# Performance work log

Hardware: AMD Instinct MI355X
Metric: run time of the kernel (lower is better)

The kernel has to match this reference:

```python
import jax, jax.numpy as jnp
import numpy as np
from jax import lax

ITER_TIME = 32
DECAY = 0.9


def setup_inputs() -> dict:
    key = jax.random.key(0)
    k1, k2, k3, k4 = jax.random.split(key, 4)
    B, D_in, N, D_out = 256, 1024, 4096, 256
    s_in = 1.0 / np.sqrt(D_in)
    s_rec = 0.5 / np.sqrt(N)  # keep recurrence stable
    s_out = 1.0 / np.sqrt(N)
    return {
        "x": jax.random.normal(k1, (B, D_in), dtype=jnp.float32),
        "W_i": jax.random.normal(k2, (D_in, N), dtype=jnp.float32) * s_in,
        "b": jnp.zeros((N,), dtype=jnp.float32),
        "W_r": jax.random.normal(k3, (N, N), dtype=jnp.float32) * s_rec,
        "W_f": jax.random.normal(k4, (N, D_out), dtype=jnp.float32) * s_out,
    }


def reference(x, W_i, b, W_r, W_f):
    # prep_input_endure: constant input drive each timestep
    i_ = x @ W_i + b  # [B, N]
    u0 = jnp.zeros_like(i_)
    r0 = jnp.zeros_like(i_)

    def step(carry, _):
        u, r = carry
        u_new = DECAY * u + i_ + r           # leaky integration of drive + recurrent feedback
        a = jax.nn.relu(u_new)               # firing rate / surrogate spike
        r_new = a @ W_r                      # recurrent N->N feedback
        f = a @ W_f                          # readout N->Y
        return (u_new, r_new), (f, u_new)

    (_, _), (fs, us) = lax.scan(step, (u0, r0), None, length=ITER_TIME)
    output = jnp.transpose(fs, (1, 0, 2))  # [B, T, output_num]
    act = jnp.transpose(us, (1, 0, 2))     # [B, T, N_num]
    return output, act
```

## Files before the change

kernel.cpp:

```cpp
#include <hip/hip_runtime.h>
#include <hip/hip_bf16.h>

#define ITER_TIME 32
#define DECAY 0.9f

typedef __attribute__((ext_vector_type(8))) short short8;
typedef __attribute__((ext_vector_type(4))) float f32x4;
typedef __attribute__((ext_vector_type(4))) short short4v;
typedef unsigned short ushort_t;
typedef unsigned int u32;

__device__ __forceinline__ void gload16(const ushort_t* g, ushort_t* l) {
    __builtin_amdgcn_global_load_lds(
        (const __attribute__((address_space(1))) u32*)g,
        (__attribute__((address_space(3))) u32*)l, 16, 0, 0);
}

__global__ void conv_f32_bf16(const float* __restrict__ in,
                              __hip_bfloat16* __restrict__ out, int n) {
    int i = blockIdx.x * 256 + threadIdx.x;
    if (i < n) out[i] = __float2bfloat16(in[i]);
}

__global__ void transpose_f32_bf16(const float* __restrict__ in,
                                   __hip_bfloat16* __restrict__ out, int R,
                                   int C) {
    __shared__ float tile[32][33];
    int tx = threadIdx.x, ty = threadIdx.y;
    size_t x = blockIdx.x * 32 + tx;
    size_t y = blockIdx.y * 32 + ty;
    tile[ty][tx] = in[y * C + x];
    __syncthreads();
    size_t ox = blockIdx.y * 32 + tx;
    size_t oy = blockIdx.x * 32 + ty;
    out[oy * R + ox] = __float2bfloat16(tile[tx][ty]);
}

__global__ __launch_bounds__(256)
void gemm_wi(const ushort_t* __restrict__ A,
             const ushort_t* __restrict__ BT,
             const float* __restrict__ bias, float* __restrict__ i_,
             float* __restrict__ u, __hip_bfloat16* __restrict__ a0,
             float* __restrict__ act, int K) {
    __shared__ __attribute__((aligned(16))) ushort_t As[2][128 * 64];
    __shared__ __attribute__((aligned(16))) ushort_t Bs[2][128 * 64];

    int m0 = blockIdx.x * 128;
    int by = blockIdx.y;
    const ushort_t* Bsrc = BT + (size_t)by * 128 * K;

    int t = threadIdx.x;
    int wave = t >> 6, lane = t & 63;
    int quad = lane >> 4, l16 = lane & 15;
    int wm = (wave >> 1) * 64, wn = (wave & 1) * 64;

    int lr = lane >> 3;
    int lcol = ((lane & 7) ^ lr) << 3;
    const ushort_t* aBase = A + (size_t)(m0 + wave * 32 + lr) * K + lcol;
    const ushort_t* bBase = Bsrc + (size_t)(wave * 32 + lr) * K + lcol;

    f32x4 acc[4][4];
#pragma unroll
    for (int i = 0; i < 4; i++)
#pragma unroll
        for (int j = 0; j < 4; j++) acc[i][j] = (f32x4){0.f, 0.f, 0.f, 0.f};

    int nt = K >> 6;
    int swz = (l16 & 7) << 3;

    auto stage = [&](int buf, int kk) {
#pragma unroll
        for (int i = 0; i < 4; ++i) {
            gload16(aBase + (size_t)(i * 8) * K + kk,
                    &As[buf][(wave * 4 + i) * 512]);
            gload16(bBase + (size_t)(i * 8) * K + kk,
                    &Bs[buf][(wave * 4 + i) * 512]);
        }
    };

    stage(0, 0);
    __syncthreads();
    int cur = 0;
    for (int it = 0; it < nt; ++it) {
        if (it + 1 < nt) stage(cur ^ 1, (it + 1) * 64);
#pragma unroll
        for (int kstep = 0; kstep < 2; ++kstep) {
            int ko = kstep * 32 + quad * 8;
            int pc = ko ^ swz;
            short8 af[4], bfr[4];
#pragma unroll
            for (int i = 0; i < 4; i++)
                af[i] = *(const short8*)&As[cur][(wm + i * 16 + l16) * 64 + pc];
#pragma unroll
            for (int j = 0; j < 4; j++)
                bfr[j] = *(const short8*)&Bs[cur][(wn + j * 16 + l16) * 64 + pc];
#pragma unroll
            for (int i = 0; i < 4; i++)
#pragma unroll
                for (int j = 0; j < 4; j++)
                    acc[i][j] = __builtin_amdgcn_mfma_f32_16x16x32_bf16(
                        af[i], bfr[j], acc[i][j], 0, 0, 0);
        }
        __syncthreads();
        cur ^= 1;
    }

#pragma unroll
    for (int i = 0; i < 4; i++)
#pragma unroll
        for (int j = 0; j < 4; j++) {
            int gcol = by * 128 + wn + j * 16 + l16;
#pragma unroll
            for (int rr = 0; rr < 4; ++rr) {
                int grow = m0 + wm + i * 16 + quad * 4 + rr;
                size_t p = (size_t)grow * 4096 + gcol;
                float iv = acc[i][j][rr] + bias[gcol];
                i_[p] = iv;
                u[p] = iv;
                __builtin_nontemporal_store(
                    iv, &act[(size_t)grow * (ITER_TIME * 4096) + gcol]);
                float ar = iv > 0.f ? iv : 0.f;
                a0[p] = __float2bfloat16(ar);
            }
        }
}

template <int ONLY_F>
__global__ __launch_bounds__(256)
void gemm_step(const ushort_t* __restrict__ A,
               const ushort_t* __restrict__ BT,
               float* __restrict__ rp,
               float* __restrict__ fp) {
    const int K = 4096, klen = 1024;
    __shared__ __attribute__((aligned(16))) ushort_t As[2][128 * 64];
    __shared__ __attribute__((aligned(16))) ushort_t Bs[2][64 * 64];

    int blk = blockIdx.x;
    int by, w;
    if (ONLY_F) {
        by = 64 + (blk >> 3);
        w = blk & 7;
    } else if (blk < 512) {
        int xcd = blk & 7, bg = (blk >> 3) & 7;
        w = blk >> 6;
        by = xcd + 8 * bg;
    } else {
        int idx = blk - 512;
        by = 64 + (idx >> 3);
        w = idx & 7;
    }
    int m = w & 1, ks = w >> 1;
    int m0 = m * 128;
    const ushort_t* Bsrc = BT + (size_t)by * 64 * K;

    int tid = threadIdx.x;
    int wave = tid >> 6, lane = tid & 63;
    int quad = lane >> 4, l16 = lane & 15;
    int wm = (wave >> 1) * 64, wn = (wave & 1) * 32;

    int lr = lane >> 3;
    int lcol = ((lane & 7) ^ lr) << 3;
    const ushort_t* aBase = A + (size_t)(m0 + wave * 32 + lr) * K + lcol;
    const ushort_t* bBase = Bsrc + (size_t)(wave * 16 + lr) * K + lcol;

    f32x4 acc[4][2];
#pragma unroll
    for (int i = 0; i < 4; i++)
#pragma unroll
        for (int j = 0; j < 2; j++) acc[i][j] = (f32x4){0.f, 0.f, 0.f, 0.f};

    const int k0 = ks * klen;
    const int nt = klen >> 6;
    int swz = (l16 & 7) << 3;

    auto stage = [&](int buf, int kk) {
#pragma unroll
        for (int i = 0; i < 4; ++i)
            gload16(aBase + (size_t)(i * 8) * K + kk,
                    &As[buf][(wave * 4 + i) * 512]);
#pragma unroll
        for (int i = 0; i < 2; ++i)
            gload16(bBase + (size_t)(i * 8) * K + kk,
                    &Bs[buf][(wave * 2 + i) * 512]);
    };

    stage(0, k0);
    __syncthreads();
    int cur = 0;
    for (int it = 0; it < nt; ++it) {
        if (it + 1 < nt) stage(cur ^ 1, k0 + (it + 1) * 64);
#pragma unroll
        for (int kstep = 0; kstep < 2; ++kstep) {
            int ko = kstep * 32 + quad * 8;
            int pc = ko ^ swz;
            short8 af[4], bfr[2];
#pragma unroll
            for (int i = 0; i < 4; i++)
                af[i] = *(const short8*)&As[cur][(wm + i * 16 + l16) * 64 + pc];
#pragma unroll
            for (int j = 0; j < 2; j++)
                bfr[j] = *(const short8*)&Bs[cur][(wn + j * 16 + l16) * 64 + pc];
#pragma unroll
            for (int i = 0; i < 4; i++)
#pragma unroll
                for (int j = 0; j < 2; j++)
                    acc[i][j] = __builtin_amdgcn_mfma_f32_16x16x32_bf16(
                        af[i], bfr[j], acc[i][j], 0, 0, 0);
        }
        __syncthreads();
        cur ^= 1;
    }

#pragma unroll
    for (int i = 0; i < 4; i++)
#pragma unroll
        for (int j = 0; j < 2; j++) {
            int cl = wn + j * 16 + l16;
#pragma unroll
            for (int rr = 0; rr < 4; ++rr) {
                int grow = m0 + wm + i * 16 + quad * 4 + rr;
                float v = acc[i][j][rr];
                if (by < 64) {
                    rp[(size_t)ks * (256 * 4096) + (size_t)grow * 4096 +
                       by * 64 + cl] = v;
                } else {
                    fp[(size_t)ks * (256 * 256) + (size_t)grow * 256 +
                       (by - 64) * 64 + cl] = v;
                }
            }
        }
}

__global__ void elem_step(const float* __restrict__ i_, float* __restrict__ u,
                          __hip_bfloat16* __restrict__ a,
                          const float* __restrict__ rp,
                          const float* __restrict__ fp,
                          float* __restrict__ out, float* __restrict__ act,
                          int t, int fonly) {
    const int NU = 256 * 4096, NU4 = NU / 4;
    const int NF = 256 * 256, NF4 = NF / 4;
    int raw = blockIdx.x * 256 + threadIdx.x;
    int id4 = fonly ? (NU4 + raw) : raw;
    if (id4 >= NU4 + NF4) return;
    if (id4 < NU4) {
        int id = id4 * 4;
        int b = id >> 12, n = id & 4095;
        f32x4 s = *(const f32x4*)&i_[id];
#pragma unroll
        for (int k = 0; k < 4; ++k)
            s += __builtin_nontemporal_load(
                (const f32x4*)&rp[(size_t)k * NU + id]);
        f32x4 un = DECAY * *(const f32x4*)&u[id] + s;
        *(f32x4*)&u[id] = un;
        short4v av;
#pragma unroll
        for (int j = 0; j < 4; ++j) {
            float ar = un[j] > 0.f ? un[j] : 0.f;
            __hip_bfloat16 h = __float2bfloat16(ar);
            av[j] = *(short*)&h;
        }
        *(short4v*)&a[id] = av;
        __builtin_nontemporal_store(
            un, (f32x4*)&act[(size_t)b * (ITER_TIME * 4096) +
                             (size_t)t * 4096 + n]);
    } else {
        int id2 = (id4 - NU4) * 4;
        int b = id2 >> 8, d = id2 & 255;
        f32x4 fv = {0.f, 0.f, 0.f, 0.f};
#pragma unroll
        for (int k = 0; k < 4; ++k)
            fv += __builtin_nontemporal_load(
                (const f32x4*)&fp[(size_t)k * NF + id2]);
        __builtin_nontemporal_store(
            fv, (f32x4*)&out[(size_t)b * (ITER_TIME * 256) +
                             (size_t)(t - 1) * 256 + d]);
    }
}

extern "C" void kernel_launch(void* const* d_in, const int* in_sizes, int n_in,
                              void* d_out, int out_size, void* d_ws,
                              size_t ws_size, hipStream_t stream) {
    const float* x = (const float*)d_in[0];
    const float* Wi = (const float*)d_in[1];
    const float* bb = (const float*)d_in[2];
    const float* Wr = (const float*)d_in[3];
    const float* Wf = (const float*)d_in[4];

    float* out = (float*)d_out;
    float* act = out + (size_t)256 * ITER_TIME * 256;

    char* ws = (char*)d_ws;
    __hip_bfloat16* BT = (__hip_bfloat16*)(ws + 0x0);
    float* i_ = (float*)(ws + 0x2200000);
    float* u = (float*)(ws + 0x2600000);
    __hip_bfloat16* a = (__hip_bfloat16*)(ws + 0x2A00000);
    float* rp = (float*)(ws + 0x2C00000);
    float* fp = (float*)(ws + 0x3C00000);
    __hip_bfloat16* WiT = (__hip_bfloat16*)(ws + 0x2C00000);
    __hip_bfloat16* xb = (__hip_bfloat16*)(ws + 0x3C00000);

    conv_f32_bf16<<<1024, 256, 0, stream>>>(x, xb, 256 * 1024);
    dim3 tb(32, 32);
    transpose_f32_bf16<<<dim3(128, 32), tb, 0, stream>>>(Wi, WiT, 1024, 4096);
    transpose_f32_bf16<<<dim3(128, 128), tb, 0, stream>>>(Wr, BT, 4096, 4096);
    transpose_f32_bf16<<<dim3(8, 128), tb, 0, stream>>>(
        Wf, BT + (size_t)4096 * 4096, 4096, 256);

    gemm_wi<<<dim3(2, 32), 256, 0, stream>>>((const ushort_t*)xb,
                                             (const ushort_t*)WiT, bb, i_, u,
                                             a, act, 1024);

    for (int t = 0; t < ITER_TIME - 1; ++t) {
        gemm_step<0><<<544, 256, 0, stream>>>((const ushort_t*)a,
                                              (const ushort_t*)BT, rp, fp);
        elem_step<<<1088, 256, 0, stream>>>(i_, u, a, rp, fp, out, act, t + 1,
                                            0);
    }
    gemm_step<1><<<32, 256, 0, stream>>>((const ushort_t*)a,
                                         (const ushort_t*)BT, rp, fp);
    elem_step<<<64, 256, 0, stream>>>(i_, u, a, rp, fp, out, act, ITER_TIME,
                                      1);
}
```

Baseline: 1.110 ms.

## Fuse recurrent GEMM with elementwise update using in-block split-K reduction

Replaces the separate GEMM (4-way split-K writing fp32 partials to global) and elementwise kernel with one fused kernel per timestep. Each block now computes a 32x64 tile with a 2-way split-K across waves, reduces through shared memory, and applies the leaky update, ReLU, bf16 conversion, act store and readout store directly. Activations are ping-ponged between two buffers to avoid read/write races. This removes the partial-sum global traffic and half the kernel launches, at the cost of smaller tiles with less operand reuse and more B-matrix reloads per block.

```diff
diff --git a/kernel.cpp b/kernel.cpp
--- a/kernel.cpp
+++ b/kernel.cpp
@@ -6,7 +6,6 @@
 
 typedef __attribute__((ext_vector_type(8))) short short8;
 typedef __attribute__((ext_vector_type(4))) float f32x4;
-typedef __attribute__((ext_vector_type(4))) short short4v;
 typedef unsigned short ushort_t;
 typedef unsigned int u32;
 
@@ -127,61 +126,62 @@
 
 template <int ONLY_F>
 __global__ __launch_bounds__(256)
-void gemm_step(const ushort_t* __restrict__ A,
-               const ushort_t* __restrict__ BT,
-               float* __restrict__ rp,
-               float* __restrict__ fp) {
-    const int K = 4096, klen = 1024;
-    __shared__ __attribute__((aligned(16))) ushort_t As[2][128 * 64];
-    __shared__ __attribute__((aligned(16))) ushort_t Bs[2][64 * 64];
+void step_fused(const ushort_t* __restrict__ A,
+                const ushort_t* __restrict__ BT,
+                const float* __restrict__ i_, float* __restrict__ u,
+                __hip_bfloat16* __restrict__ a_out,
+                float* __restrict__ out, float* __restrict__ act,
+                const int t) {
+    const int K = 4096;
+    __shared__ __attribute__((aligned(16))) ushort_t As[2][2][32 * 64];
+    __shared__ __attribute__((aligned(16))) ushort_t Bs[2][2][64 * 64];
 
     int blk = blockIdx.x;
-    int by, w;
+    int mt, by;
     if (ONLY_F) {
+        mt = blk & 7;
         by = 64 + (blk >> 3);
-        w = blk & 7;
     } else if (blk < 512) {
-        int xcd = blk & 7, bg = (blk >> 3) & 7;
-        w = blk >> 6;
-        by = xcd + 8 * bg;
+        int xcd = blk & 7, g = blk >> 3;
+        by = xcd + 8 * (g & 7);
+        mt = g >> 3;
     } else {
         int idx = blk - 512;
         by = 64 + (idx >> 3);
-        w = idx & 7;
-    }
-    int m = w & 1, ks = w >> 1;
-    int m0 = m * 128;
+        mt = idx & 7;
+    }
+    int m0 = mt * 32;
     const ushort_t* Bsrc = BT + (size_t)by * 64 * K;
 
     int tid = threadIdx.x;
     int wave = tid >> 6, lane = tid & 63;
+    int kg = wave >> 1, ng = wave & 1;
     int quad = lane >> 4, l16 = lane & 15;
-    int wm = (wave >> 1) * 64, wn = (wave & 1) * 32;
-
     int lr = lane >> 3;
     int lcol = ((lane & 7) ^ lr) << 3;
-    const ushort_t* aBase = A + (size_t)(m0 + wave * 32 + lr) * K + lcol;
-    const ushort_t* bBase = Bsrc + (size_t)(wave * 16 + lr) * K + lcol;
-
-    f32x4 acc[4][2];
-#pragma unroll
-    for (int i = 0; i < 4; i++)
+
+    const ushort_t* aBase = A + (size_t)(m0 + ng * 16 + lr) * K + lcol;
+    const ushort_t* bBase = Bsrc + (size_t)(ng * 32 + lr) * K + lcol;
+
+    f32x4 acc[2][2];
+#pragma unroll
+    for (int i = 0; i < 2; i++)
 #pragma unroll
         for (int j = 0; j < 2; j++) acc[i][j] = (f32x4){0.f, 0.f, 0.f, 0.f};
 
-    const int k0 = ks * klen;
-    const int nt = klen >> 6;
+    const int k0 = kg * 2048;
+    const int nt = 32;
     int swz = (l16 & 7) << 3;
 
     auto stage = [&](int buf, int kk) {
 #pragma unroll
+        for (int i = 0; i < 2; ++i)
+            gload16(aBase + (size_t)(i * 8) * K + kk,
+                    &As[kg][buf][(ng * 2 + i) * 512]);
+#pragma unroll
         for (int i = 0; i < 4; ++i)
-            gload16(aBase + (size_t)(i * 8) * K + kk,
-                    &As[buf][(wave * 4 + i) * 512]);
-#pragma unroll
-        for (int i = 0; i < 2; ++i)
             gload16(bBase + (size_t)(i * 8) * K + kk,
-                    &Bs[buf][(wave * 2 + i) * 512]);
+                    &Bs[kg][buf][(ng * 4 + i) * 512]);
     };
 
     stage(0, k0);
@@ -193,15 +193,16 @@
         for (int kstep = 0; kstep < 2; ++kstep) {
             int ko = kstep * 32 + quad * 8;
             int pc = ko ^ swz;
-            short8 af[4], bfr[2];
-#pragma unroll
-            for (int i = 0; i < 4; i++)
-                af[i] = *(const short8*)&As[cur][(wm + i * 16 + l16) * 64 + pc];
+            short8 af[2], bfr[2];
+#pragma unroll
+            for (int i = 0; i < 2; i++)
+                af[i] = *(const short8*)&As[kg][cur][(i * 16 + l16) * 64 + pc];
 #pragma unroll
             for (int j = 0; j < 2; j++)
-                bfr[j] = *(const short8*)&Bs[cur][(wn + j * 16 + l16) * 64 + pc];
-#pragma unroll
-            for (int i = 0; i < 4; i++)
+                bfr[j] = *(const short8*)&Bs[kg][cur]
+                                            [(ng * 32 + j * 16 + l16) * 64 + pc];
+#pragma unroll
+            for (int i = 0; i < 2; i++)
 #pragma unroll
                 for (int j = 0; j < 2; j++)
                     acc[i][j] = __builtin_amdgcn_mfma_f32_16x16x32_bf16(
@@ -211,69 +212,56 @@
         cur ^= 1;
     }
 
-#pragma unroll
-    for (int i = 0; i < 4; i++)
-#pragma unroll
-        for (int j = 0; j < 2; j++) {
-            int cl = wn + j * 16 + l16;
-#pragma unroll
-            for (int rr = 0; rr < 4; ++rr) {
-                int grow = m0 + wm + i * 16 + quad * 4 + rr;
-                float v = acc[i][j][rr];
-                if (by < 64) {
-                    rp[(size_t)ks * (256 * 4096) + (size_t)grow * 4096 +
-                       by * 64 + cl] = v;
-                } else {
-                    fp[(size_t)ks * (256 * 256) + (size_t)grow * 256 +
-                       (by - 64) * 64 + cl] = v;
+    f32x4* red = (f32x4*)&As[0][0][0];
+    if (kg == 1) {
+#pragma unroll
+        for (int i = 0; i < 2; i++)
+#pragma unroll
+            for (int j = 0; j < 2; j++)
+                red[(size_t)(ng * 64 + lane) * 4 + (i * 2 + j)] = acc[i][j];
+    }
+    __syncthreads();
+    if (kg != 0) return;
+#pragma unroll
+    for (int i = 0; i < 2; i++)
+#pragma unroll
+        for (int j = 0; j < 2; j++)
+            acc[i][j] += red[(size_t)(ng * 64 + lane) * 4 + (i * 2 + j)];
+
+    if (by < 64) {
+#pragma unroll
+        for (int i = 0; i < 2; i++)
+#pragma unroll
+            for (int j = 0; j < 2; j++) {
+                int gcol = by * 64 + ng * 32 + j * 16 + l16;
+#pragma unroll
+                for (int rr = 0; rr < 4; ++rr) {
+                    int grow = m0 + i * 16 + quad * 4 + rr;
+                    size_t p = (size_t)grow * 4096 + gcol;
+                    float un = DECAY * u[p] + i_[p] + acc[i][j][rr];
+                    u[p] = un;
+                    __builtin_nontemporal_store(
+                        un, &act[(size_t)grow * (ITER_TIME * 4096) +
+                                 (size_t)(t + 1) * 4096 + gcol]);
+                    float ar = un > 0.f ? un : 0.f;
+                    a_out[p] = __float2bfloat16(ar);
                 }
             }
-        }
-}
-
-__global__ void elem_step(const float* __restrict__ i_, float* __restrict__ u,
-                          __hip_bfloat16* __restrict__ a,
-                          const float* __restrict__ rp,
-                          const float* __restrict__ fp,
-                          float* __restrict__ out, float* __restrict__ act,
-                          int t, int fonly) {
-    const int NU = 256 * 4096, NU4 = NU / 4;
-    const int NF = 256 * 256, NF4 = NF / 4;
-    int raw = blockIdx.x * 256 + threadIdx.x;
-    int id4 = fonly ? (NU4 + raw) : raw;
-    if (id4 >= NU4 + NF4) return;
-    if (id4 < NU4) {
-        int id = id4 * 4;
-        int b = id >> 12, n = id & 4095;
-        f32x4 s = *(const f32x4*)&i_[id];
-#pragma unroll
-        for (int k = 0; k < 4; ++k)
-            s += __builtin_nontemporal_load(
-                (const f32x4*)&rp[(size_t)k * NU + id]);
-        f32x4 un = DECAY * *(const f32x4*)&u[id] + s;
-        *(f32x4*)&u[id] = un;
-        short4v av;
-#pragma unroll
-        for (int j = 0; j < 4; ++j) {
-            float ar = un[j] > 0.f ? un[j] : 0.f;
-            __hip_bfloat16 h = __float2bfloat16(ar);
-            av[j] = *(short*)&h;
-        }
-        *(short4v*)&a[id] = av;
-        __builtin_nontemporal_store(
-            un, (f32x4*)&act[(size_t)b * (ITER_TIME * 4096) +
-                             (size_t)t * 4096 + n]);
     } else {
-        int id2 = (id4 - NU4) * 4;
-        int b = id2 >> 8, d = id2 & 255;
-        f32x4 fv = {0.f, 0.f, 0.f, 0.f};
-#pragma unroll
-        for (int k = 0; k < 4; ++k)
-            fv += __builtin_nontemporal_load(
-                (const f32x4*)&fp[(size_t)k * NF + id2]);
-        __builtin_nontemporal_store(
-            fv, (f32x4*)&out[(size_t)b * (ITER_TIME * 256) +
-                             (size_t)(t - 1) * 256 + d]);
+#pragma unroll
+        for (int i = 0; i < 2; i++)
+#pragma unroll
+            for (int j = 0; j < 2; j++) {
+                int c2 = (by - 64) * 64 + ng * 32 + j * 16 + l16;
+#pragma unroll
+                for (int rr = 0; rr < 4; ++rr) {
+                    int grow = m0 + i * 16 + quad * 4 + rr;
+                    __builtin_nontemporal_store(
+                        acc[i][j][rr],
+                        &out[(size_t)grow * (ITER_TIME * 256) +
+                             (size_t)t * 256 + c2]);
+                }
+            }
     }
 }
 
@@ -293,11 +281,10 @@
     __hip_bfloat16* BT = (__hip_bfloat16*)(ws + 0x0);
     float* i_ = (float*)(ws + 0x2200000);
     float* u = (float*)(ws + 0x2600000);
-    __hip_bfloat16* a = (__hip_bfloat16*)(ws + 0x2A00000);
-    float* rp = (float*)(ws + 0x2C00000);
-    float* fp = (float*)(ws + 0x3C00000);
-    __hip_bfloat16* WiT = (__hip_bfloat16*)(ws + 0x2C00000);
-    __hip_bfloat16* xb = (__hip_bfloat16*)(ws + 0x3C00000);
+    __hip_bfloat16* a0 = (__hip_bfloat16*)(ws + 0x2A00000);
+    __hip_bfloat16* a1 = (__hip_bfloat16*)(ws + 0x2C00000);
+    __hip_bfloat16* WiT = (__hip_bfloat16*)(ws + 0x2E00000);
+    __hip_bfloat16* xb = (__hip_bfloat16*)(ws + 0x3600000);
 
     conv_f32_bf16<<<1024, 256, 0, stream>>>(x, xb, 256 * 1024);
     dim3 tb(32, 32);
@@ -308,16 +295,15 @@
 
     gemm_wi<<<dim3(2, 32), 256, 0, stream>>>((const ushort_t*)xb,
                                              (const ushort_t*)WiT, bb, i_, u,
-                                             a, act, 1024);
+                                             a0, act, 1024);
 
     for (int t = 0; t < ITER_TIME - 1; ++t) {
-        gemm_step<0><<<544, 256, 0, stream>>>((const ushort_t*)a,
-                                              (const ushort_t*)BT, rp, fp);
-        elem_step<<<1088, 256, 0, stream>>>(i_, u, a, rp, fp, out, act, t + 1,
-                                            0);
-    }
-    gemm_step<1><<<32, 256, 0, stream>>>((const ushort_t*)a,
-                                         (const ushort_t*)BT, rp, fp);
-    elem_step<<<64, 256, 0, stream>>>(i_, u, a, rp, fp, out, act, ITER_TIME,
-                                      1);
-}
+        const ushort_t* ain = (const ushort_t*)((t & 1) ? a1 : a0);
+        __hip_bfloat16* aout = (t & 1) ? a0 : a1;
+        step_fused<0><<<544, 256, 0, stream>>>(ain, (const ushort_t*)BT, i_, u,
+                                               aout, out, act, t);
+    }
+    step_fused<1><<<32, 256, 0, stream>>>((const ushort_t*)a1,
+                                          (const ushort_t*)BT, i_, u, a0, out,
+                                          act, ITER_TIME - 1);
+}
```

After: 1.151 ms. 1.04x slower.
